# Kernel tuning notes

Measured on AMD Instinct MI355X. Metric: run time of the kernel, lower is better.

Reference implementation:

```python
import jax, jax.numpy as jnp
import numpy as np

N_QUBITS = 14
D = 2 ** N_QUBITS            # 16384 state dim
E = 2048                     # embedding_dim
N_PAIRS = N_QUBITS * (N_QUBITS - 1) // 2  # 91


def _linear_init(key, fan_in, fan_out):
    kw, kb = jax.random.split(key)
    bound = 1.0 / np.sqrt(fan_in)
    w = jax.random.uniform(kw, (fan_in, fan_out), jnp.float32, -bound, bound)
    b = jax.random.uniform(kb, (fan_out,), jnp.float32, -bound, bound)
    return w, b


def setup_inputs() -> dict:
    key = jax.random.key(0)
    ks = jax.random.split(key, 12)
    qs_real = jax.random.normal(ks[0], (D,), jnp.float32) * 0.1
    qs_imag = jax.random.normal(ks[1], (D,), jnp.float32) * 0.1
    amp_w1, amp_b1 = _linear_init(ks[2], 2 * D, E)
    amp_w2, amp_b2 = _linear_init(ks[3], E, E)
    ln_g = jnp.ones((E,), jnp.float32)
    ln_b = jnp.zeros((E,), jnp.float32)
    ph_w1, ph_b1 = _linear_init(ks[4], D, E // 2)
    ph_w2, ph_b2 = _linear_init(ks[5], E // 2, E // 2)
    ent_w1, ent_b1 = _linear_init(ks[6], N_PAIRS, E // 4)
    ent_w2, ent_b2 = _linear_init(ks[7], E // 4, E // 4)
    fus_w, fus_b = _linear_init(ks[8], E + E // 2 + E // 4, E)
    return dict(qs_real=qs_real, qs_imag=qs_imag,
                amp_w1=amp_w1, amp_b1=amp_b1, amp_w2=amp_w2, amp_b2=amp_b2,
                ln_g=ln_g, ln_b=ln_b,
                ph_w1=ph_w1, ph_b1=ph_b1, ph_w2=ph_w2, ph_b2=ph_b2,
                ent_w1=ent_w1, ent_b1=ent_b1, ent_w2=ent_w2, ent_b2=ent_b2,
                fus_w=fus_w, fus_b=fus_b, n_qubits=N_QUBITS)


def _layer_norm(x, g, b, eps=1e-5):
    m = jnp.mean(x)
    v = jnp.mean(jnp.square(x - m))
    return (x - m) / jnp.sqrt(v + eps) * g + b


def _entanglement_features(re, im, n_qubits):
    # abs(sum(state[::2^(n-i-1)] * state[1::2^(n-j-1)])) for all pairs i<j,
    # slices truncated to common length 2^(i+1); complex arithmetic via re/im.
    feats = []
    for i in range(n_qubits):
        si = 2 ** (n_qubits - i - 1)
        L = 2 ** (i + 1)
        a, b = re[::si], im[::si]          # length 2^(i+1)
        for j in range(i + 1, n_qubits):
            sj = 2 ** (n_qubits - j - 1)
            c, d = re[1::sj][:L], im[1::sj][:L]
            rr = jnp.sum(a * c - b * d)
            ii = jnp.sum(a * d + b * c)
            feats.append(jnp.sqrt(rr * rr + ii * ii))
    return jnp.stack(feats)


def reference(qs_real, qs_imag,
              amp_w1, amp_b1, amp_w2, amp_b2, ln_g, ln_b,
              ph_w1, ph_b1, ph_w2, ph_b2,
              ent_w1, ent_b1, ent_w2, ent_b2,
              fus_w, fus_b, n_qubits):
    # normalize the complex state
    norm = jnp.sqrt(jnp.sum(qs_real * qs_real + qs_imag * qs_imag))
    re = qs_real / norm
    im = qs_imag / norm
    phases = jnp.arctan2(im, re)
    # amplitude encoder on [real; imag]
    x = jnp.concatenate([re, im])
    a = jax.nn.relu(x @ amp_w1 + amp_b1) @ amp_w2 + amp_b2
    amp_emb = _layer_norm(a, ln_g, ln_b)
    # phase encoder
    ph_emb = jax.nn.relu(phases @ ph_w1 + ph_b1) @ ph_w2 + ph_b2
    # entanglement encoder
    ef = _entanglement_features(re, im, int(n_qubits))
    ent_emb = jax.nn.relu(ef @ ent_w1 + ent_b1) @ ent_w2 + ent_b2
    combined = jnp.concatenate([amp_emb, ph_emb, ent_emb])
    return combined @ fus_w + fus_b
```

## Files before the change

kernel.cpp:

```cpp
#include <hip/hip_runtime.h>
#include <math.h>

#define DD 16384
#define NQ 14

__device__ __forceinline__ void atomAddF(float* p, float v) {
#if defined(__HIP_PLATFORM_AMD__)
    unsafeAtomicAdd(p, v);
#else
    atomicAdd(p, v);
#endif
}

__global__ __launch_bounds__(256) void k_norm(const float4* __restrict__ qr4,
                                              const float4* __restrict__ qi4,
                                              float* __restrict__ sum) {
    __shared__ float sred[4];
    int t = blockIdx.x * 256 + threadIdx.x;
    float4 r = qr4[t], m = qi4[t];
    float v = r.x * r.x + r.y * r.y + r.z * r.z + r.w * r.w +
              m.x * m.x + m.y * m.y + m.z * m.z + m.w * m.w;
#pragma unroll
    for (int off = 32; off; off >>= 1) v += __shfl_down(v, off);
    if ((threadIdx.x & 63) == 0) sred[threadIdx.x >> 6] = v;
    __syncthreads();
    if (threadIdx.x == 0) atomAddF(sum, sred[0] + sred[1] + sred[2] + sred[3]);
}

__global__ __launch_bounds__(256) void k_prep(const float4* __restrict__ qr4,
                                              const float4* __restrict__ qi4,
                                              const float* __restrict__ sum,
                                              float4* __restrict__ x4,
                                              float4* __restrict__ ph4) {
    int t = blockIdx.x * 256 + threadIdx.x;
    float inv = 1.0f / sqrtf(*sum);
    float4 r = qr4[t], m = qi4[t];
    float4 xr = {r.x * inv, r.y * inv, r.z * inv, r.w * inv};
    float4 xi = {m.x * inv, m.y * inv, m.z * inv, m.w * inv};
    x4[t] = xr;
    x4[DD / 4 + t] = xi;
    float4 p = {atan2f(m.x, r.x), atan2f(m.y, r.y), atan2f(m.z, r.z), atan2f(m.w, r.w)};
    ph4[t] = p;
}

__global__ __launch_bounds__(512, 4) void k_matvec(const float* __restrict__ W,
                                                   const float* __restrict__ xpre,
                                                   const float* __restrict__ xbias, int act,
                                                   float* __restrict__ acc,
                                                   const float* __restrict__ obias,
                                                   int C4, int R, int rpc) {
    __shared__ float sx[128];
    int chunk = blockIdx.x;
    int r0 = chunk * rpc;
    int nr = min(rpc, R - r0);
    for (int i = threadIdx.x; i < nr; i += blockDim.x) {
        float v = xpre[r0 + i];
        if (act) v = fmaxf(v + xbias[r0 + i], 0.0f);
        sx[i] = v;
    }
    __syncthreads();
    const float4* __restrict__ Wp =
        reinterpret_cast<const float4*>(W) + (size_t)r0 * C4 + threadIdx.x;
    float ax = 0.f, ay = 0.f, az = 0.f, aw = 0.f;
    float bx = 0.f, by = 0.f, bz = 0.f, bw = 0.f;
    int i = 0;
    for (; i + 8 <= nr; i += 8) {
        float4 w0 = Wp[0];
        float4 w1 = Wp[(size_t)C4 * 1];
        float4 w2 = Wp[(size_t)C4 * 2];
        float4 w3 = Wp[(size_t)C4 * 3];
        float4 w4 = Wp[(size_t)C4 * 4];
        float4 w5 = Wp[(size_t)C4 * 5];
        float4 w6 = Wp[(size_t)C4 * 6];
        float4 w7 = Wp[(size_t)C4 * 7];
        float x0 = sx[i + 0], x1 = sx[i + 1], x2 = sx[i + 2], x3 = sx[i + 3];
        float x4 = sx[i + 4], x5 = sx[i + 5], x6 = sx[i + 6], x7 = sx[i + 7];
        ax = fmaf(x0, w0.x, ax); ay = fmaf(x0, w0.y, ay); az = fmaf(x0, w0.z, az); aw = fmaf(x0, w0.w, aw);
        bx = fmaf(x1, w1.x, bx); by = fmaf(x1, w1.y, by); bz = fmaf(x1, w1.z, bz); bw = fmaf(x1, w1.w, bw);
        ax = fmaf(x2, w2.x, ax); ay = fmaf(x2, w2.y, ay); az = fmaf(x2, w2.z, az); aw = fmaf(x2, w2.w, aw);
        bx = fmaf(x3, w3.x, bx); by = fmaf(x3, w3.y, by); bz = fmaf(x3, w3.z, bz); bw = fmaf(x3, w3.w, bw);
        ax = fmaf(x4, w4.x, ax); ay = fmaf(x4, w4.y, ay); az = fmaf(x4, w4.z, az); aw = fmaf(x4, w4.w, aw);
        bx = fmaf(x5, w5.x, bx); by = fmaf(x5, w5.y, by); bz = fmaf(x5, w5.z, bz); bw = fmaf(x5, w5.w, bw);
        ax = fmaf(x6, w6.x, ax); ay = fmaf(x6, w6.y, ay); az = fmaf(x6, w6.z, az); aw = fmaf(x6, w6.w, aw);
        bx = fmaf(x7, w7.x, bx); by = fmaf(x7, w7.y, by); bz = fmaf(x7, w7.z, bz); bw = fmaf(x7, w7.w, bw);
        Wp += (size_t)C4 * 8;
    }
    for (; i < nr; i++) {
        float4 w = *Wp;
        Wp += C4;
        float xv = sx[i];
        ax = fmaf(xv, w.x, ax); ay = fmaf(xv, w.y, ay);
        az = fmaf(xv, w.z, az); aw = fmaf(xv, w.w, aw);
    }
    ax += bx; ay += by; az += bz; aw += bw;
    int col = threadIdx.x * 4;
    if (chunk == 0 && obias) {
        ax += obias[col + 0]; ay += obias[col + 1];
        az += obias[col + 2]; aw += obias[col + 3];
    }
    atomAddF(&acc[col + 0], ax);
    atomAddF(&acc[col + 1], ay);
    atomAddF(&acc[col + 2], az);
    atomAddF(&acc[col + 3], aw);
}

__global__ __launch_bounds__(512) void k_ln(const float* __restrict__ a,
                                            const float* __restrict__ b2,
                                            const float* __restrict__ g,
                                            const float* __restrict__ bb,
                                            float* __restrict__ out) {
    __shared__ float s1[8], s2[8];
    int tid = threadIdx.x;
    float v[4];
    float s = 0.f;
#pragma unroll
    for (int e = 0; e < 4; e++) {
        int idx = tid + 512 * e;
        v[e] = a[idx] + b2[idx];
        s += v[e];
    }
#pragma unroll
    for (int off = 32; off; off >>= 1) s += __shfl_down(s, off);
    if ((tid & 63) == 0) s1[tid >> 6] = s;
    __syncthreads();
    float tot = s1[0] + s1[1] + s1[2] + s1[3] + s1[4] + s1[5] + s1[6] + s1[7];
    float mean = tot * (1.0f / 2048.0f);
    float q = 0.f;
#pragma unroll
    for (int e = 0; e < 4; e++) {
        float d = v[e] - mean;
        q += d * d;
    }
#pragma unroll
    for (int off = 32; off; off >>= 1) q += __shfl_down(q, off);
    if ((tid & 63) == 0) s2[tid >> 6] = q;
    __syncthreads();
    float tv = s2[0] + s2[1] + s2[2] + s2[3] + s2[4] + s2[5] + s2[6] + s2[7];
    float var = tv * (1.0f / 2048.0f);
    float inv = 1.0f / sqrtf(var + 1e-5f);
#pragma unroll
    for (int e = 0; e < 4; e++) {
        int idx = tid + 512 * e;
        out[idx] = (v[e] - mean) * inv * g[idx] + bb[idx];
    }
}

__global__ __launch_bounds__(512) void k_ent(const float* __restrict__ x,
                                             const float* __restrict__ w1,
                                             const float* __restrict__ b1,
                                             const float* __restrict__ w2,
                                             const float* __restrict__ b2,
                                             float* __restrict__ out) {
    __shared__ float s_ef[96];
    __shared__ float s_h[512];
    int tid = threadIdx.x;
    int wave = tid >> 6, lane = tid & 63;
    const float* re = x;
    const float* im = x + DD;
    for (int p = wave; p < 91; p += 8) {
        int i = 0, rem = p;
        while (rem >= (NQ - 1) - i) { rem -= (NQ - 1) - i; i++; }
        int j = i + 1 + rem;
        int si = 1 << (NQ - i - 1);
        int sj = 1 << (NQ - j - 1);
        int L = 1 << (i + 1);
        float rr = 0.f, ii = 0.f;
        for (int k = lane; k < L; k += 64) {
            float a = re[k * si], b = im[k * si];
            float c = re[1 + k * sj], d = im[1 + k * sj];
            rr += a * c - b * d;
            ii += a * d + b * c;
        }
#pragma unroll
        for (int off = 32; off; off >>= 1) {
            rr += __shfl_down(rr, off);
            ii += __shfl_down(ii, off);
        }
        if (lane == 0) s_ef[p] = sqrtf(rr * rr + ii * ii);
    }
    __syncthreads();
    float h = b1[tid];
    for (int p = 0; p < 91; p++) h = fmaf(s_ef[p], w1[p * 512 + tid], h);
    s_h[tid] = fmaxf(h, 0.f);
    __syncthreads();
    float o = b2[tid];
    for (int k = 0; k < 512; k++) o = fmaf(s_h[k], w2[k * 512 + tid], o);
    out[tid] = o;
}

extern "C" void kernel_launch(void* const* d_in, const int* in_sizes, int n_in,
                              void* d_out, int out_size, void* d_ws, size_t ws_size,
                              hipStream_t stream) {
    const float* qs_real = (const float*)d_in[0];
    const float* qs_imag = (const float*)d_in[1];
    const float* amp_w1  = (const float*)d_in[2];
    const float* amp_b1  = (const float*)d_in[3];
    const float* amp_w2  = (const float*)d_in[4];
    const float* amp_b2  = (const float*)d_in[5];
    const float* ln_g    = (const float*)d_in[6];
    const float* ln_b    = (const float*)d_in[7];
    const float* ph_w1   = (const float*)d_in[8];
    const float* ph_b1   = (const float*)d_in[9];
    const float* ph_w2   = (const float*)d_in[10];
    const float* ph_b2   = (const float*)d_in[11];
    const float* ent_w1  = (const float*)d_in[12];
    const float* ent_b1  = (const float*)d_in[13];
    const float* ent_w2  = (const float*)d_in[14];
    const float* ent_b2  = (const float*)d_in[15];
    const float* fus_w   = (const float*)d_in[16];
    const float* fus_b   = (const float*)d_in[17];
    float* out = (float*)d_out;
    float* ws = (float*)d_ws;

    const int o_sum  = 0;
    const int o_h1   = 1024;
    const int o_a    = 4096;
    const int o_p1   = 8192;
    const int o_comb = 16384;
    const int o_x    = 20480;
    const int o_ph   = 53248;

    hipMemsetAsync(d_ws, 0, (size_t)(o_comb + 3584) * sizeof(float), stream);
    hipMemsetAsync(d_out, 0, 2048 * sizeof(float), stream);

    k_norm<<<16, 256, 0, stream>>>((const float4*)qs_real, (const float4*)qs_imag, ws + o_sum);
    k_prep<<<16, 256, 0, stream>>>((const float4*)qs_real, (const float4*)qs_imag,
                                   ws + o_sum, (float4*)(ws + o_x), (float4*)(ws + o_ph));

    k_matvec<<<256, 512, 0, stream>>>(amp_w1, ws + o_x, nullptr, 0, ws + o_h1, nullptr,
                                      512, 2 * DD, 128);
    k_matvec<<<256, 512, 0, stream>>>(amp_w2, ws + o_h1, amp_b1, 1, ws + o_a, nullptr,
                                      512, 2048, 8);
    k_ln<<<1, 512, 0, stream>>>(ws + o_a, amp_b2, ln_g, ln_b, ws + o_comb);

    k_matvec<<<512, 256, 0, stream>>>(ph_w1, ws + o_ph, nullptr, 0, ws + o_p1, nullptr,
                                      256, DD, 32);
    k_matvec<<<256, 256, 0, stream>>>(ph_w2, ws + o_p1, ph_b1, 1, ws + o_comb + 2048, ph_b2,
                                      256, 1024, 4);

    k_ent<<<1, 512, 0, stream>>>(ws + o_x, ent_w1, ent_b1, ent_w2, ent_b2,
                                 ws + o_comb + 3072);

    k_matvec<<<256, 512, 0, stream>>>(fus_w, ws + o_comb, nullptr, 0, out, fus_b,
                                      512, 3584, 14);
}
```

Measured before the change: 690.4 us.

## Split entanglement encoder into per-pair feature blocks plus generic matvec kernels

Replaces the single-block entanglement kernel with a 91-block feature kernel, one block per qubit pair, followed by two k_matvec launches for the two dense layers. The old kernel ran the whole encoder, including a serial 512-step loop per thread, on one workgroup and so serialized on one compute unit. The new layout spreads the work across many CUs at the cost of two extra kernel launches and workspace round trips. Correctness depends on k_matvec's split-K accumulation into zeroed workspace (o_ef and o_eh1 lie inside the memset region) and on its bias/relu handling.

```diff
diff --git a/kernel.cpp b/kernel.cpp
--- a/kernel.cpp
+++ b/kernel.cpp
@@ -145,47 +145,40 @@
     }
 }
 
-__global__ __launch_bounds__(512) void k_ent(const float* __restrict__ x,
-                                             const float* __restrict__ w1,
-                                             const float* __restrict__ b1,
-                                             const float* __restrict__ w2,
-                                             const float* __restrict__ b2,
-                                             float* __restrict__ out) {
-    __shared__ float s_ef[96];
-    __shared__ float s_h[512];
-    int tid = threadIdx.x;
-    int wave = tid >> 6, lane = tid & 63;
+__global__ __launch_bounds__(256) void k_efeat(const float* __restrict__ x,
+                                               float* __restrict__ ef) {
+    __shared__ float srr[4], sii[4];
+    int p = blockIdx.x;
+    int i = 0, rem = p;
+    while (rem >= (NQ - 1) - i) { rem -= (NQ - 1) - i; i++; }
+    int j = i + 1 + rem;
+    int si = 1 << (NQ - i - 1);
+    int sj = 1 << (NQ - j - 1);
+    int L = 1 << (i + 1);
     const float* re = x;
     const float* im = x + DD;
-    for (int p = wave; p < 91; p += 8) {
-        int i = 0, rem = p;
-        while (rem >= (NQ - 1) - i) { rem -= (NQ - 1) - i; i++; }
-        int j = i + 1 + rem;
-        int si = 1 << (NQ - i - 1);
-        int sj = 1 << (NQ - j - 1);
-        int L = 1 << (i + 1);
-        float rr = 0.f, ii = 0.f;
-        for (int k = lane; k < L; k += 64) {
-            float a = re[k * si], b = im[k * si];
-            float c = re[1 + k * sj], d = im[1 + k * sj];
-            rr += a * c - b * d;
-            ii += a * d + b * c;
-        }
-#pragma unroll
-        for (int off = 32; off; off >>= 1) {
-            rr += __shfl_down(rr, off);
-            ii += __shfl_down(ii, off);
-        }
-        if (lane == 0) s_ef[p] = sqrtf(rr * rr + ii * ii);
-    }
-    __syncthreads();
-    float h = b1[tid];
-    for (int p = 0; p < 91; p++) h = fmaf(s_ef[p], w1[p * 512 + tid], h);
-    s_h[tid] = fmaxf(h, 0.f);
-    __syncthreads();
-    float o = b2[tid];
-    for (int k = 0; k < 512; k++) o = fmaf(s_h[k], w2[k * 512 + tid], o);
-    out[tid] = o;
+    float rr = 0.f, ii = 0.f;
+    for (int k = threadIdx.x; k < L; k += 256) {
+        float a = re[k * si], b = im[k * si];
+        float c = re[1 + k * sj], d = im[1 + k * sj];
+        rr += a * c - b * d;
+        ii += a * d + b * c;
+    }
+#pragma unroll
+    for (int off = 32; off; off >>= 1) {
+        rr += __shfl_down(rr, off);
+        ii += __shfl_down(ii, off);
+    }
+    if ((threadIdx.x & 63) == 0) {
+        srr[threadIdx.x >> 6] = rr;
+        sii[threadIdx.x >> 6] = ii;
+    }
+    __syncthreads();
+    if (threadIdx.x == 0) {
+        float R = srr[0] + srr[1] + srr[2] + srr[3];
+        float I = sii[0] + sii[1] + sii[2] + sii[3];
+        ef[p] = sqrtf(R * R + I * I);
+    }
 }
 
 extern "C" void kernel_launch(void* const* d_in, const int* in_sizes, int n_in,
@@ -216,6 +209,8 @@
     const int o_h1   = 1024;
     const int o_a    = 4096;
     const int o_p1   = 8192;
+    const int o_ef   = 12288;
+    const int o_eh1  = 13312;
     const int o_comb = 16384;
     const int o_x    = 20480;
     const int o_ph   = 53248;
@@ -238,8 +233,11 @@
     k_matvec<<<256, 256, 0, stream>>>(ph_w2, ws + o_p1, ph_b1, 1, ws + o_comb + 2048, ph_b2,
                                       256, 1024, 4);
 
-    k_ent<<<1, 512, 0, stream>>>(ws + o_x, ent_w1, ent_b1, ent_w2, ent_b2,
-                                 ws + o_comb + 3072);
+    k_efeat<<<91, 256, 0, stream>>>(ws + o_x, ws + o_ef);
+    k_matvec<<<4, 128, 0, stream>>>(ent_w1, ws + o_ef, nullptr, 0, ws + o_eh1, nullptr,
+                                    128, 91, 23);
+    k_matvec<<<16, 128, 0, stream>>>(ent_w2, ws + o_eh1, ent_b1, 1, ws + o_comb + 3072, ent_b2,
+                                     128, 512, 32);
 
     k_matvec<<<256, 512, 0, stream>>>(fus_w, ws + o_comb, nullptr, 0, out, fus_b,
                                       512, 3584, 14);
```

Result: faster. 637.6 us (-7.6%).
